# Optimization experiments

Hardware: AMD Instinct MI355X
Metric: run time of the kernel (lower is better)

Reference implementation:

```python
import math
import jax, jax.numpy as jnp
import numpy as np

T_LEN, BSZ, E_DIM, N_HEADS = 2048, 4, 768, 12


def setup_inputs() -> dict:
    key = jax.random.key(0)
    k0, k1, k2 = jax.random.split(key, 3)
    E = E_DIM
    return {
        "query": jax.random.normal(k0, (T_LEN, BSZ, E), dtype=jnp.float32),
        "attn_mask": jnp.zeros((T_LEN, T_LEN), dtype=jnp.float32),
        "in_proj_weight": jax.random.normal(k1, (3 * E, E), dtype=jnp.float32) * (1.0 / math.sqrt(E)),
        "in_proj_bias": jnp.zeros((3 * E,), dtype=jnp.float32),
        "out_proj_weight": jax.random.normal(k2, (E, E), dtype=jnp.float32) * (1.0 / math.sqrt(E)),
        "out_proj_bias": jnp.zeros((E,), dtype=jnp.float32),
        "num_heads": N_HEADS,
    }


def _rope_tables(seq_len, head_dim, dtype):
    # position_enc[pos, j] = pos / 10000**(2j/head_dim), j in [0, head_dim//2)
    pos = jnp.arange(seq_len, dtype=jnp.float32)[:, None]
    j = jnp.arange(head_dim // 2, dtype=jnp.float32)[None, :]
    ang = pos / jnp.power(jnp.float32(10000.0), 2.0 * j / head_dim)
    # stack([x, x], -1).reshape == repeat-interleave by 2 along last dim
    sin = jnp.repeat(jnp.sin(ang), 2, axis=-1).astype(dtype)  # (S, hd)
    cos = jnp.repeat(jnp.cos(ang), 2, axis=-1).astype(dtype)
    return sin, cos


def _rotate_half(x):
    # interleaved pairs: (x0, x1, x2, x3, ...) -> (-x1, x0, -x3, x2, ...)
    x_even = x[..., 0::2]
    x_odd = x[..., 1::2]
    return jnp.stack([-x_odd, x_even], axis=-1).reshape(x.shape)


def reference(query, attn_mask, in_proj_weight, in_proj_bias, out_proj_weight, out_proj_bias, num_heads):
    T, B, E = query.shape
    H = num_heads
    hd = E // H

    # fused QKV in-projection: (T, B, 3E)
    proj = jnp.einsum('tbe,fe->tbf', query, in_proj_weight) + in_proj_bias
    q, k, v = jnp.split(proj, 3, axis=-1)  # each (T, B, E)

    def to_bhtd(x):
        return jnp.transpose(x.reshape(T, B, H, hd), (1, 2, 0, 3))  # (B, H, T, hd)

    q, k, v = to_bhtd(q), to_bhtd(k), to_bhtd(v)

    sin, cos = _rope_tables(T, hd, q.dtype)  # (T, hd), broadcast over (B, H)
    q = q * cos + _rotate_half(q) * sin
    k = k * cos + _rotate_half(k) * sin

    scale = 1.0 / math.sqrt(hd)
    scores = jnp.einsum('bhtd,bhsd->bhts', q, k) * scale + attn_mask[None, None, :, :]
    attn = jax.nn.softmax(scores, axis=-1)
    out = jnp.einsum('bhts,bhsd->bhtd', attn, v)  # (B, H, T, hd)

    out = jnp.transpose(out, (2, 0, 1, 3)).reshape(T * B, E)  # (T*B, E)
    out = out @ out_proj_weight.T + out_proj_bias
    return out.reshape(T, B, E)
```

## Files before the change

kernel.cpp:

```cpp
#include <hip/hip_runtime.h>
#include <math.h>

#define TLEN 2048
#define BSZ  4
#define EDIM 768
#define NH   12
#define HD   64
#define NBH  (BSZ * NH)

typedef __bf16 bf16;
typedef __bf16 bf16x8 __attribute__((ext_vector_type(8)));
typedef float  f32x4  __attribute__((ext_vector_type(4)));
typedef unsigned int uint;

__device__ __forceinline__ f32x4 mfma16(bf16x8 a, bf16x8 b, f32x4 c) {
  return __builtin_amdgcn_mfma_f32_16x16x32_bf16(a, b, c, 0, 0, 0);
}

#define GLD16(gp, lp)                                                          \
  __builtin_amdgcn_global_load_lds(                                            \
      (const __attribute__((address_space(1))) uint32_t*)(gp),                 \
      (__attribute__((address_space(3))) uint32_t*)(lp), 16, 0, 0)

__device__ __forceinline__ bf16x8 ldsfrag(const bf16* t, int row, int kb) {
  return *reinterpret_cast<const bf16x8*>(
      (const char*)t + row * 128 + (kb ^ ((row & 7) << 4)));
}

#define CT_OFF   0x0u
#define ST_OFF   0x40000u
#define FLG_OFF  0x80000u
#define AQ_OFF   0x100000u
#define VT_OFF   0x100000u
#define QB_OFF   0xD00000u
#define KB_OFF   0x1900000u
#define VB_OFF   0x2500000u
#define XB_OFF   0x2500000u
#define WI_OFF   0x3100000u
#define WO_OFF   0x3460000u

#define QN8  786432
#define WIN8 221184
#define WON8 73728

__device__ __forceinline__ void cvt8(const float* __restrict__ s,
                                     bf16* __restrict__ d, int i) {
  const float4* sp = reinterpret_cast<const float4*>(s) + (size_t)i * 2;
  float4 a = sp[0], b = sp[1];
  bf16x8 o;
  o[0] = (bf16)a.x; o[1] = (bf16)a.y; o[2] = (bf16)a.z; o[3] = (bf16)a.w;
  o[4] = (bf16)b.x; o[5] = (bf16)b.y; o[6] = (bf16)b.z; o[7] = (bf16)b.w;
  reinterpret_cast<bf16x8*>(d)[i] = o;
}

__global__ __launch_bounds__(256) void prep_all_kernel(
    const float* __restrict__ q, bf16* __restrict__ qo,
    const float* __restrict__ wi, bf16* __restrict__ wio,
    const float* __restrict__ wo, bf16* __restrict__ woo,
    const float* __restrict__ mask, uint* __restrict__ flags,
    float* __restrict__ ct, float* __restrict__ st) {
  int bid = blockIdx.x;
  int tid = threadIdx.x;
  if (bid < 256) {
    int i = bid * 256 + tid;
    int t = i >> 5, j = i & 31;
    double ang = (double)t * pow(10000.0, -(double)j / 32.0);
    st[i] = (float)sin(ang);
    ct[i] = (float)cos(ang);
  } else if (bid < 4480) {
    int i = (bid - 256) * 256 + tid;
    if (i < QN8) { cvt8(q, qo, i); return; }
    int j = i - QN8;
    if (j < WIN8) { cvt8(wi, wio, j); return; }
    cvt8(wo, woo, j - WIN8);
  } else {
    int tile = bid - 4480;
    int ty = tile >> 5, tx = tile & 31;
    uint acc = 0;
#pragma unroll
    for (int i = 0; i < 4; ++i) {
      int c = tid + 256 * i;
      int rr = c >> 4, cc = (c & 15) * 4;
      float4 v = *reinterpret_cast<const float4*>(
          mask + (size_t)(ty * 64 + rr) * TLEN + tx * 64 + cc);
      acc |= __float_as_uint(v.x) | __float_as_uint(v.y) |
             __float_as_uint(v.z) | __float_as_uint(v.w);
    }
    unsigned long long b = __ballot(acc != 0);
    __shared__ uint red[4];
    if ((tid & 63) == 0) red[tid >> 6] = (b != 0ull) ? 1u : 0u;
    __syncthreads();
    if (tid == 0) flags[tile] = red[0] | red[1] | red[2] | red[3];
  }
}

__global__ __launch_bounds__(256) void vtrans_kernel(const bf16* __restrict__ v,
                                                     bf16* __restrict__ vt) {
  int w = threadIdx.x >> 6, lane = threadIdx.x & 63;
  int bh = blockIdx.y;
  int t0 = (blockIdx.x * 4 + w) * 64;
  const bf16* src = v + ((size_t)bh * TLEN + t0) * HD;
  bf16* dst = vt + (size_t)bh * HD * TLEN + t0;
  int d0 = (lane & 7) * 8, tr = (lane >> 3) * 8;
  bf16x8 in[8];
#pragma unroll
  for (int r = 0; r < 8; ++r)
    in[r] = *reinterpret_cast<const bf16x8*>(src + (size_t)(tr + r) * HD + d0);
  bf16x8 out[8];
#pragma unroll
  for (int j = 0; j < 8; ++j)
#pragma unroll
    for (int r = 0; r < 8; ++r) out[j][r] = in[r][j];
#pragma unroll
  for (int j = 0; j < 8; ++j)
    *reinterpret_cast<bf16x8*>(dst + (size_t)(d0 + j) * TLEN + tr) = out[j];
}

template <int MODE>
__global__ __launch_bounds__(256) void gemm_bt(
    const bf16* __restrict__ A, const bf16* __restrict__ B,
    const float* __restrict__ bias,
    const float* __restrict__ ct, const float* __restrict__ st,
    bf16* __restrict__ qo, bf16* __restrict__ ko, bf16* __restrict__ vo,
    float* __restrict__ fo) {
  constexpr int K = EDIM;
  __shared__ __align__(16) bf16 As[128 * 64];
  __shared__ __align__(16) bf16 Bs[128 * 64];
  int tid = threadIdx.x;
  int lane = tid & 63, w = tid >> 6;
  int wr = w >> 1, wc = w & 1;
  int g = lane >> 4, cl = lane & 15;
  int bm = blockIdx.y, bn = blockIdx.x;
  int lrow = lane >> 3;
  int colb = ((lane & 7) ^ lrow) << 4;
  const char* Abase = (const char*)(A + (size_t)bm * 128 * K);
  const char* Bbase = (const char*)(B + (size_t)bn * 128 * K);

  f32x4 acc[4][4] = {};

  for (int kt = 0; kt < K; kt += 64) {
#pragma unroll
    for (int i = 0; i < 4; ++i) {
      int qi = w * 4 + i;
      int row = qi * 8 + lrow;
      GLD16(Abase + (size_t)row * (K * 2) + kt * 2 + colb, As + qi * 512 + lane * 8);
      GLD16(Bbase + (size_t)row * (K * 2) + kt * 2 + colb, Bs + qi * 512 + lane * 8);
    }
    __syncthreads();
#pragma unroll
    for (int kk = 0; kk < 2; ++kk) {
      bf16x8 af[4], bfr[4];
#pragma unroll
      for (int mi = 0; mi < 4; ++mi)
        af[mi] = ldsfrag(As, wr * 64 + mi * 16 + cl, kk * 64 + g * 16);
#pragma unroll
      for (int ni = 0; ni < 4; ++ni)
        bfr[ni] = ldsfrag(Bs, wc * 64 + ni * 16 + cl, kk * 64 + g * 16);
#pragma unroll
      for (int mi = 0; mi < 4; ++mi)
#pragma unroll
        for (int ni = 0; ni < 4; ++ni)
          acc[mi][ni] = mfma16(af[mi], bfr[ni], acc[mi][ni]);
    }
    __syncthreads();
  }

  if (MODE == 0) {
#pragma unroll
    for (int mi = 0; mi < 4; ++mi) {
      int mbase = bm * 128 + wr * 64 + mi * 16 + 4 * g;
      int t = mbase >> 2;
#pragma unroll
      for (int ni = 0; ni < 4; ++ni) {
        int f = bn * 128 + wc * 64 + ni * 16 + cl;
        int sec = f / EDIM;
        int f0 = f - sec * EDIM;
        int h = f0 >> 6, d = f0 & 63;
        float bv = bias[f];
        float vals[4];
#pragma unroll
        for (int r = 0; r < 4; ++r) vals[r] = acc[mi][ni][r] + bv;
        if (sec < 2) {
          int j = d >> 1;
          float cv = ct[t * 32 + j], sv = st[t * 32 + j];
          bf16* dst = (sec == 0) ? qo : ko;
#pragma unroll
          for (int r = 0; r < 4; ++r) {
            float other = __shfl_xor(vals[r], 1);
            float rv = (d & 1) ? (vals[r] * cv + other * sv)
                               : (vals[r] * cv - other * sv);
            if (sec == 0) rv *= 0.125f;
            dst[(((size_t)r * NH + h) * TLEN + t) * HD + d] = (bf16)rv;
          }
        } else {
#pragma unroll
          for (int r = 0; r < 4; ++r)
            vo[(((size_t)r * NH + h) * TLEN + t) * HD + d] = (bf16)vals[r];
        }
      }
    }
  } else {
#pragma unroll
    for (int mi = 0; mi < 4; ++mi) {
      int mbase = bm * 128 + wr * 64 + mi * 16 + 4 * g;
#pragma unroll
      for (int ni = 0; ni < 4; ++ni) {
        int n = bn * 128 + wc * 64 + ni * 16 + cl;
        float bv = bias[n];
#pragma unroll
        for (int r = 0; r < 4; ++r)
          fo[(size_t)(mbase + r) * EDIM + n] = acc[mi][ni][r] + bv;
      }
    }
  }
}

__global__ __launch_bounds__(512) void attn_kernel(
    const bf16* __restrict__ qa, const bf16* __restrict__ ka,
    const bf16* __restrict__ vt, const float* __restrict__ mask,
    const uint* __restrict__ flags, bf16* __restrict__ xo) {
  __shared__ __align__(16) bf16 Ks[2][4096];
  __shared__ __align__(16) bf16 Vs[2][4096];
  __shared__ __align__(16) bf16 Ps[8][16][72];
  int tid = threadIdx.x;
  int lane = tid & 63, w = tid >> 6;
  int g = lane >> 4, cl = lane & 15;
  int bh = blockIdx.y;
  int qrow0 = blockIdx.x * 128 + w * 16;
  const bf16* qbh = qa + (size_t)bh * TLEN * HD;
  const char* kbase = (const char*)(ka + (size_t)bh * TLEN * HD);
  const char* vbase = (const char*)(vt + (size_t)bh * HD * TLEN);
  int lrow = lane >> 3;
  int colb = ((lane & 7) ^ lrow) << 4;
  int sw = w & 3;

  bf16x8 qf[2];
#pragma unroll
  for (int h = 0; h < 2; ++h)
    qf[h] = *reinterpret_cast<const bf16x8*>(
        qbh + (size_t)(qrow0 + cl) * HD + h * 32 + g * 8);

  bf16x8 ones;
#pragma unroll
  for (int j = 0; j < 8; ++j) ones[j] = (bf16)1.0f;

  f32x4 o[5] = {};
  float mrow[4];
#pragma unroll
  for (int r = 0; r < 4; ++r) mrow[r] = -1e30f;

  {
#pragma unroll
    for (int i = 0; i < 2; ++i) {
      int qi = sw * 2 + i;
      int row = qi * 8 + lrow;
      if (w < 4)
        GLD16(kbase + (size_t)row * 128 + colb, &Ks[0][qi * 512 + lane * 8]);
      else
        GLD16(vbase + (size_t)row * (TLEN * 2) + colb, &Vs[0][qi * 512 + lane * 8]);
    }
  }
  __syncthreads();

  for (int stile = 0; stile < TLEN / 64; ++stile) {
    int cur = stile & 1;
    if (stile + 1 < TLEN / 64) {
      int s1 = (stile + 1) * 64;
#pragma unroll
      for (int i = 0; i < 2; ++i) {
        int qi = sw * 2 + i;
        int row = qi * 8 + lrow;
        if (w < 4)
          GLD16(kbase + (size_t)(s1 + row) * 128 + colb,
                &Ks[cur ^ 1][qi * 512 + lane * 8]);
        else
          GLD16(vbase + (size_t)row * (TLEN * 2) + s1 * 2 + colb,
                &Vs[cur ^ 1][qi * 512 + lane * 8]);
      }
    }
    const bf16* Kc = Ks[cur];
    const bf16* Vc = Vs[cur];

    f32x4 sc[4];
#pragma unroll
    for (int ni = 0; ni < 4; ++ni) {
      bf16x8 k0 = ldsfrag(Kc, ni * 16 + cl, g * 16);
      bf16x8 k1 = ldsfrag(Kc, ni * 16 + cl, 64 + g * 16);
      f32x4 z = {};
      z = mfma16(qf[0], k0, z);
      z = mfma16(qf[1], k1, z);
      sc[ni] = z;
    }

    if (flags[(qrow0 >> 6) * 32 + stile]) {
#pragma unroll
      for (int ni = 0; ni < 4; ++ni)
#pragma unroll
        for (int r = 0; r < 4; ++r)
          sc[ni][r] += mask[(size_t)(qrow0 + 4 * g + r) * TLEN +
                            stile * 64 + ni * 16 + cl];
    }

    float ml[4];
#pragma unroll
    for (int r = 0; r < 4; ++r)
      ml[r] = fmaxf(fmaxf(sc[0][r], sc[1][r]), fmaxf(sc[2][r], sc[3][r]));
    bool ok = (ml[0] <= mrow[0] + 8.f) && (ml[1] <= mrow[1] + 8.f) &&
              (ml[2] <= mrow[2] + 8.f) && (ml[3] <= mrow[3] + 8.f);
    if (!__all(ok)) {
#pragma unroll
      for (int r = 0; r < 4; ++r) {
        float m0 = ml[r];
#pragma unroll
        for (int off = 1; off < 16; off <<= 1) m0 = fmaxf(m0, __shfl_xor(m0, off));
        float mn = fmaxf(mrow[r], m0);
        float al = __expf(mrow[r] - mn);
        mrow[r] = mn;
#pragma unroll
        for (int di = 0; di < 5; ++di) o[di][r] *= al;
      }
    }

#pragma unroll
    for (int ni = 0; ni < 4; ++ni)
#pragma unroll
      for (int r = 0; r < 4; ++r)
        Ps[w][4 * g + r][ni * 16 + cl] = (bf16)__expf(sc[ni][r] - mrow[r]);
    bf16x8 pf0 = *reinterpret_cast<const bf16x8*>(&Ps[w][cl][g * 8]);
    bf16x8 pf1 = *reinterpret_cast<const bf16x8*>(&Ps[w][cl][32 + g * 8]);

#pragma unroll
    for (int di = 0; di < 4; ++di) {
      bf16x8 v0 = ldsfrag(Vc, di * 16 + cl, g * 16);
      bf16x8 v1 = ldsfrag(Vc, di * 16 + cl, 64 + g * 16);
      o[di] = mfma16(pf0, v0, o[di]);
      o[di] = mfma16(pf1, v1, o[di]);
    }
    o[4] = mfma16(pf0, ones, o[4]);
    o[4] = mfma16(pf1, ones, o[4]);

    __syncthreads();
  }

  int b = bh / NH, h = bh % NH;
#pragma unroll
  for (int di = 0; di < 4; ++di)
#pragma unroll
    for (int r = 0; r < 4; ++r) {
      int t = qrow0 + 4 * g + r;
      float val = o[di][r] / o[4][r];
      xo[(size_t)(t * BSZ + b) * EDIM + h * HD + di * 16 + cl] = (bf16)val;
    }
}

extern "C" void kernel_launch(void* const* d_in, const int* in_sizes, int n_in,
                              void* d_out, int out_size, void* d_ws, size_t ws_size,
                              hipStream_t stream) {
  const float* query = (const float*)d_in[0];
  const float* mask  = (const float*)d_in[1];
  const float* win   = (const float*)d_in[2];
  const float* bin   = (const float*)d_in[3];
  const float* wout  = (const float*)d_in[4];
  const float* bout  = (const float*)d_in[5];
  (void)in_sizes; (void)n_in; (void)out_size; (void)ws_size;

  char* ws = (char*)d_ws;
  float* ct   = (float*)(ws + CT_OFF);
  float* st   = (float*)(ws + ST_OFF);
  uint*  flg  = (uint*)(ws + FLG_OFF);
  bf16*  aq   = (bf16*)(ws + AQ_OFF);
  bf16*  vtb  = (bf16*)(ws + VT_OFF);
  bf16*  qb   = (bf16*)(ws + QB_OFF);
  bf16*  kb   = (bf16*)(ws + KB_OFF);
  bf16*  vb   = (bf16*)(ws + VB_OFF);
  bf16*  xb   = (bf16*)(ws + XB_OFF);
  bf16*  wib  = (bf16*)(ws + WI_OFF);
  bf16*  wob  = (bf16*)(ws + WO_OFF);
  float* out  = (float*)d_out;

  prep_all_kernel<<<dim3(5504), dim3(256), 0, stream>>>(
      query, aq, win, wib, wout, wob, mask, flg, ct, st);

  gemm_bt<0><<<dim3(3 * EDIM / 128, TLEN * BSZ / 128), dim3(256), 0, stream>>>(
      aq, wib, bin, ct, st, qb, kb, vb, nullptr);

  vtrans_kernel<<<dim3(TLEN / 256, NBH), dim3(256), 0, stream>>>(vb, vtb);

  attn_kernel<<<dim3(TLEN / 128, NBH), dim3(512), 0, stream>>>(
      qb, kb, vtb, mask, flg, xb);

  gemm_bt<1><<<dim3(EDIM / 128, TLEN * BSZ / 128), dim3(256), 0, stream>>>(
      xb, wob, bout, nullptr, nullptr, nullptr, nullptr, nullptr, out);
}
```

Baseline: 280.2 us.

## Transpose attention MFMA operands to keep P in registers and use exp2

Swaps the MFMA operand order so score tiles come out transposed, with each lane owning one query row. The P matrix can then be packed straight into bf16 registers with v_cvt_pk_bf16_f32 and fed to the PV MFMA without going through LDS. LOG2E is folded into the Q scaling and mask so exp2f replaces __expf, and the row max becomes one value per lane with fewer shuffles. The V fragment loads are split into 64-bit pieces so the k-ordering matches the new P layout, and the output store is vectorised; this relies on that permuted ordering being consistent.

```diff
diff --git a/kernel.cpp b/kernel.cpp
--- a/kernel.cpp
+++ b/kernel.cpp
@@ -7,6 +7,7 @@
 #define NH   12
 #define HD   64
 #define NBH  (BSZ * NH)
+#define LOG2E 1.44269504088896f
 
 typedef __bf16 bf16;
 typedef __bf16 bf16x8 __attribute__((ext_vector_type(8)));
@@ -17,6 +18,12 @@
   return __builtin_amdgcn_mfma_f32_16x16x32_bf16(a, b, c, 0, 0, 0);
 }
 
+__device__ __forceinline__ uint cvtpk(float lo, float hi) {
+  uint r;
+  asm("v_cvt_pk_bf16_f32 %0, %1, %2" : "=v"(r) : "v"(lo), "v"(hi));
+  return r;
+}
+
 #define GLD16(gp, lp)                                                          \
   __builtin_amdgcn_global_load_lds(                                            \
       (const __attribute__((address_space(1))) uint32_t*)(gp),                 \
@@ -24,6 +31,11 @@
 
 __device__ __forceinline__ bf16x8 ldsfrag(const bf16* t, int row, int kb) {
   return *reinterpret_cast<const bf16x8*>(
+      (const char*)t + row * 128 + (kb ^ ((row & 7) << 4)));
+}
+
+__device__ __forceinline__ uint2 ldsfrag64(const bf16* t, int row, int kb) {
+  return *reinterpret_cast<const uint2*>(
       (const char*)t + row * 128 + (kb ^ ((row & 7) << 4)));
 }
 
@@ -189,7 +201,7 @@
             float other = __shfl_xor(vals[r], 1);
             float rv = (d & 1) ? (vals[r] * cv + other * sv)
                                : (vals[r] * cv - other * sv);
-            if (sec == 0) rv *= 0.125f;
+            if (sec == 0) rv *= 0.125f * LOG2E;
             dst[(((size_t)r * NH + h) * TLEN + t) * HD + d] = (bf16)rv;
           }
         } else {
@@ -221,7 +233,6 @@
     const uint* __restrict__ flags, bf16* __restrict__ xo) {
   __shared__ __align__(16) bf16 Ks[2][4096];
   __shared__ __align__(16) bf16 Vs[2][4096];
-  __shared__ __align__(16) bf16 Ps[8][16][72];
   int tid = threadIdx.x;
   int lane = tid & 63, w = tid >> 6;
   int g = lane >> 4, cl = lane & 15;
@@ -233,6 +244,7 @@
   int lrow = lane >> 3;
   int colb = ((lane & 7) ^ lrow) << 4;
   int sw = w & 3;
+  const uint* flgrow = flags + (qrow0 >> 6) * 32;
 
   bf16x8 qf[2];
 #pragma unroll
@@ -244,21 +256,18 @@
 #pragma unroll
   for (int j = 0; j < 8; ++j) ones[j] = (bf16)1.0f;
 
-  f32x4 o[5] = {};
-  float mrow[4];
-#pragma unroll
-  for (int r = 0; r < 4; ++r) mrow[r] = -1e30f;
-
-  {
-#pragma unroll
-    for (int i = 0; i < 2; ++i) {
-      int qi = sw * 2 + i;
-      int row = qi * 8 + lrow;
-      if (w < 4)
-        GLD16(kbase + (size_t)row * 128 + colb, &Ks[0][qi * 512 + lane * 8]);
-      else
-        GLD16(vbase + (size_t)row * (TLEN * 2) + colb, &Vs[0][qi * 512 + lane * 8]);
-    }
+  f32x4 o[4] = {};
+  f32x4 oden = {};
+  float mrow = -1e30f;
+
+#pragma unroll
+  for (int i = 0; i < 2; ++i) {
+    int qi = sw * 2 + i;
+    int row = qi * 8 + lrow;
+    if (w < 4)
+      GLD16(kbase + (size_t)row * 128 + colb, &Ks[0][qi * 512 + lane * 8]);
+    else
+      GLD16(vbase + (size_t)row * (TLEN * 2) + colb, &Vs[0][qi * 512 + lane * 8]);
   }
   __syncthreads();
 
@@ -287,70 +296,81 @@
       bf16x8 k0 = ldsfrag(Kc, ni * 16 + cl, g * 16);
       bf16x8 k1 = ldsfrag(Kc, ni * 16 + cl, 64 + g * 16);
       f32x4 z = {};
-      z = mfma16(qf[0], k0, z);
-      z = mfma16(qf[1], k1, z);
+      z = mfma16(k0, qf[0], z);
+      z = mfma16(k1, qf[1], z);
       sc[ni] = z;
     }
 
-    if (flags[(qrow0 >> 6) * 32 + stile]) {
+    if (flgrow[stile]) {
+      int q = qrow0 + cl;
 #pragma unroll
       for (int ni = 0; ni < 4; ++ni)
 #pragma unroll
         for (int r = 0; r < 4; ++r)
-          sc[ni][r] += mask[(size_t)(qrow0 + 4 * g + r) * TLEN +
-                            stile * 64 + ni * 16 + cl];
-    }
-
-    float ml[4];
-#pragma unroll
-    for (int r = 0; r < 4; ++r)
-      ml[r] = fmaxf(fmaxf(sc[0][r], sc[1][r]), fmaxf(sc[2][r], sc[3][r]));
-    bool ok = (ml[0] <= mrow[0] + 8.f) && (ml[1] <= mrow[1] + 8.f) &&
-              (ml[2] <= mrow[2] + 8.f) && (ml[3] <= mrow[3] + 8.f);
-    if (!__all(ok)) {
-#pragma unroll
-      for (int r = 0; r < 4; ++r) {
-        float m0 = ml[r];
-#pragma unroll
-        for (int off = 1; off < 16; off <<= 1) m0 = fmaxf(m0, __shfl_xor(m0, off));
-        float mn = fmaxf(mrow[r], m0);
-        float al = __expf(mrow[r] - mn);
-        mrow[r] = mn;
-#pragma unroll
-        for (int di = 0; di < 5; ++di) o[di][r] *= al;
-      }
-    }
-
-#pragma unroll
-    for (int ni = 0; ni < 4; ++ni)
-#pragma unroll
-      for (int r = 0; r < 4; ++r)
-        Ps[w][4 * g + r][ni * 16 + cl] = (bf16)__expf(sc[ni][r] - mrow[r]);
-    bf16x8 pf0 = *reinterpret_cast<const bf16x8*>(&Ps[w][cl][g * 8]);
-    bf16x8 pf1 = *reinterpret_cast<const bf16x8*>(&Ps[w][cl][32 + g * 8]);
+          sc[ni][r] = fmaf(mask[(size_t)q * TLEN + stile * 64 + ni * 16 + 4 * g + r],
+                           LOG2E, sc[ni][r]);
+    }
+
+    float ml = fmaxf(fmaxf(fmaxf(sc[0][0], sc[0][1]), fmaxf(sc[0][2], sc[0][3])),
+                     fmaxf(fmaxf(sc[1][0], sc[1][1]), fmaxf(sc[1][2], sc[1][3])));
+    ml = fmaxf(ml,
+               fmaxf(fmaxf(fmaxf(sc[2][0], sc[2][1]), fmaxf(sc[2][2], sc[2][3])),
+                     fmaxf(fmaxf(sc[3][0], sc[3][1]), fmaxf(sc[3][2], sc[3][3]))));
+    if (!__all(ml <= mrow + 11.54f)) {
+      float mfull = fmaxf(ml, __shfl_xor(ml, 16));
+      mfull = fmaxf(mfull, __shfl_xor(mfull, 32));
+      float mn = fmaxf(mrow, mfull);
+      float al = exp2f(mrow - mn);
+      mrow = mn;
+#pragma unroll
+      for (int di = 0; di < 4; ++di)
+#pragma unroll
+        for (int r = 0; r < 4; ++r) o[di][r] *= al;
+#pragma unroll
+      for (int r = 0; r < 4; ++r) oden[r] *= al;
+    }
+
+    union { uint u[4]; bf16x8 v; } f0, f1;
+#pragma unroll
+    for (int ni = 0; ni < 4; ++ni) {
+      float p0 = exp2f(sc[ni][0] - mrow);
+      float p1 = exp2f(sc[ni][1] - mrow);
+      float p2 = exp2f(sc[ni][2] - mrow);
+      float p3 = exp2f(sc[ni][3] - mrow);
+      uint lo = cvtpk(p0, p1);
+      uint hi2 = cvtpk(p2, p3);
+      if (ni < 2) { f0.u[2 * ni] = lo; f0.u[2 * ni + 1] = hi2; }
+      else        { f1.u[2 * (ni - 2)] = lo; f1.u[2 * (ni - 2) + 1] = hi2; }
+    }
 
 #pragma unroll
     for (int di = 0; di < 4; ++di) {
-      bf16x8 v0 = ldsfrag(Vc, di * 16 + cl, g * 16);
-      bf16x8 v1 = ldsfrag(Vc, di * 16 + cl, 64 + g * 16);
-      o[di] = mfma16(pf0, v0, o[di]);
-      o[di] = mfma16(pf1, v1, o[di]);
-    }
-    o[4] = mfma16(pf0, ones, o[4]);
-    o[4] = mfma16(pf1, ones, o[4]);
+      int row = di * 16 + cl;
+      union { uint2 h[2]; bf16x8 v; } va, vb;
+      va.h[0] = ldsfrag64(Vc, row, 8 * g);
+      va.h[1] = ldsfrag64(Vc, row, 32 + 8 * g);
+      vb.h[0] = ldsfrag64(Vc, row, 64 + 8 * g);
+      vb.h[1] = ldsfrag64(Vc, row, 96 + 8 * g);
+      o[di] = mfma16(va.v, f0.v, o[di]);
+      o[di] = mfma16(vb.v, f1.v, o[di]);
+    }
+    oden = mfma16(ones, f0.v, oden);
+    oden = mfma16(ones, f1.v, oden);
 
     __syncthreads();
   }
 
   int b = bh / NH, h = bh % NH;
-#pragma unroll
-  for (int di = 0; di < 4; ++di)
-#pragma unroll
-    for (int r = 0; r < 4; ++r) {
-      int t = qrow0 + 4 * g + r;
-      float val = o[di][r] / o[4][r];
-      xo[(size_t)(t * BSZ + b) * EDIM + h * HD + di * 16 + cl] = (bf16)val;
-    }
+  int t = qrow0 + cl;
+  float inv = 1.0f / oden[0];
+  bf16* dst = xo + (size_t)(t * BSZ + b) * EDIM + h * HD + 4 * g;
+#pragma unroll
+  for (int di = 0; di < 4; ++di) {
+    union { bf16 hh[4]; uint2 u; } w4;
+#pragma unroll
+    for (int r = 0; r < 4; ++r) w4.hh[r] = (bf16)(o[di][r] * inv);
+    *reinterpret_cast<uint2*>(dst + di * 16) = w4.u;
+  }
 }
 
 extern "C" void kernel_launch(void* const* d_in, const int* in_sizes, int n_in,
```

Measured after the change: 290.0 us. 3.5% more time.
